# Kernel tuning notes

Measured on AMD Instinct MI355X. Metric: run time of the kernel, lower is better.

## Reference

```python
import jax, jax.numpy as jnp
import numpy as np

N_FFT = 2048
HOP = 512
N_FREQ = N_FFT // 2 + 1  # 1025


def _dft_conv_weights():
    # periodic ('fftbins=True') Hann window, matching librosa get_window('hann', N, fftbins=True)
    n = np.arange(N_FFT)
    win = 0.5 - 0.5 * np.cos(2.0 * np.pi * n / N_FFT)
    k = np.arange(N_FREQ)
    ang = 2.0 * np.pi * np.outer(k, n) / N_FFT  # (F, n_fft)
    # W[n, k] = exp(-2*pi*i*n*k/N); real part = cos, imag part = -sin; windowed per-tap
    w_real = (np.cos(ang) * win[None, :]).astype(np.float32)
    w_imag = (-np.sin(ang) * win[None, :]).astype(np.float32)
    return w_real, w_imag


def setup_inputs() -> dict:
    key = jax.random.key(0)
    x = jax.random.normal(key, (16, 320000), dtype=jnp.float32)
    w_real, w_imag = _dft_conv_weights()
    return {
        "input": x,
        "conv_real_w": jnp.asarray(w_real),
        "conv_imag_w": jnp.asarray(w_imag),
    }


def reference(input, conv_real_w, conv_imag_w):
    # center=True: reflect-pad n_fft//2 on both sides
    pad = N_FFT // 2
    x = jnp.pad(input, ((0, 0), (pad, pad)), mode="reflect")  # (B, L + n_fft)
    L = x.shape[1]
    T = (L - N_FFT) // HOP + 1  # time_steps
    # frame extraction == Conv1d with kernel n_fft, stride hop
    idx = jnp.arange(T)[:, None] * HOP + jnp.arange(N_FFT)[None, :]  # (T, n_fft)
    frames = x[:, idx]  # (B, T, n_fft)
    real = jnp.einsum("btn,fn->bft", frames, conv_real_w)  # (B, F, T)
    imag = jnp.einsum("btn,fn->bft", frames, conv_imag_w)  # (B, F, T)
    return real, imag
```

## Files before the change

kernel.cpp:

```cpp
#include <hip/hip_runtime.h>

#define B_BATCH 16
#define XLEN    320000
#define NFFT    2048
#define HOP     512
#define PADW    1024
#define NFREQ   1025
#define T_OUT   626
#define M_ROWS  2050
#define BM      128
#define BN      128
#define BK      64
#define MT      17
#define NTT     5
#define KT      32

#define XPAD_LEN    322048
#define XPAD_STRIDE 330240
#define APACK_BYTES ((size_t)MT * KT * 16384)
#define XPAD_BYTES  ((size_t)B_BATCH * XPAD_STRIDE * 2)
#define WS_NEEDED   (APACK_BYTES + XPAD_BYTES)

typedef __bf16 bf16x8 __attribute__((ext_vector_type(8)));
typedef __bf16 bf16x4 __attribute__((ext_vector_type(4)));
typedef float  f32x4  __attribute__((ext_vector_type(4)));

__device__ __forceinline__ unsigned lds_off(int row, int kbyte) {
    return (unsigned)(row * 128 + (kbyte ^ ((row & 7) << 4)));
}

__device__ __forceinline__ void gload_lds16(const void* g, void* l) {
    __builtin_amdgcn_global_load_lds(
        (const __attribute__((address_space(1))) unsigned int*)g,
        (__attribute__((address_space(3))) unsigned int*)l,
        16, 0, 0);
}

__global__ __launch_bounds__(256) void prep_w(
    const float* __restrict__ wre, const float* __restrict__ wim,
    __bf16* __restrict__ apack)
{
    const int gid  = blockIdx.x * 256 + threadIdx.x;
    const int slot = gid & 7;
    const int row  = (gid >> 3) & 127;
    const int kt   = (gid >> 10) & 31;
    const int mt   = gid >> 15;

    const int grow = mt * 128 + row;
    const int k    = kt * 64 + (slot ^ (row & 7)) * 8;

    bf16x8 v;
    if (grow < M_ROWS) {
        const float* src = (grow < NFREQ)
            ? (wre + (size_t)grow * NFFT + k)
            : (wim + (size_t)(grow - NFREQ) * NFFT + k);
        const float4 a = *reinterpret_cast<const float4*>(src);
        const float4 b = *reinterpret_cast<const float4*>(src + 4);
        v[0] = (__bf16)a.x; v[1] = (__bf16)a.y; v[2] = (__bf16)a.z; v[3] = (__bf16)a.w;
        v[4] = (__bf16)b.x; v[5] = (__bf16)b.y; v[6] = (__bf16)b.z; v[7] = (__bf16)b.w;
    } else {
        v = bf16x8{};
    }
    *reinterpret_cast<bf16x8*>(apack + ((size_t)(mt * KT + kt) * 8192 + row * 64 + slot * 8)) = v;
}

__global__ __launch_bounds__(256) void prep_x(
    const float* __restrict__ x, __bf16* __restrict__ xpad)
{
    const int gid = blockIdx.x * 256 + threadIdx.x;
    const int b   = gid / (XPAD_STRIDE / 8);
    const int i0  = (gid % (XPAD_STRIDE / 8)) * 8;
    const float* xb = x + (size_t)b * XLEN;

    bf16x8 v;
    const int pos0 = i0 - PADW;
    if (pos0 >= 0 && pos0 + 8 <= XLEN) {
        const float4 a = *reinterpret_cast<const float4*>(xb + pos0);
        const float4 c = *reinterpret_cast<const float4*>(xb + pos0 + 4);
        v[0] = (__bf16)a.x; v[1] = (__bf16)a.y; v[2] = (__bf16)a.z; v[3] = (__bf16)a.w;
        v[4] = (__bf16)c.x; v[5] = (__bf16)c.y; v[6] = (__bf16)c.z; v[7] = (__bf16)c.w;
    } else {
        #pragma unroll
        for (int e = 0; e < 8; ++e) {
            const int i = i0 + e;
            if (i >= XPAD_LEN) { v[e] = (__bf16)0.f; continue; }
            int p = i - PADW;
            p = (p < 0) ? -p : p;
            p = (p >= XLEN) ? (2 * XLEN - 2 - p) : p;
            v[e] = (__bf16)xb[p];
        }
    }
    *reinterpret_cast<bf16x8*>(xpad + (size_t)b * XPAD_STRIDE + i0) = v;
}

__global__ __launch_bounds__(256) void stft_gemm2(
    const __bf16* __restrict__ apack,
    const __bf16* __restrict__ xpad,
    float* __restrict__ out)
{
    __shared__ __align__(16) unsigned char ldsA[16384];
    __shared__ __align__(16) unsigned char ldsB[16384];

    const int tid  = threadIdx.x;
    const int lane = tid & 63;
    const int wid  = tid >> 6;
    const int wm   = wid >> 1;
    const int wn   = wid & 1;

    const int bid = blockIdx.x;
    const int b   = bid / (MT * NTT);
    const int rem = bid % (MT * NTT);
    const int mt  = rem / NTT;
    const int nt  = rem % NTT;

    const int row0 = mt * BM;
    const int col0 = nt * BN;

    const char* atiles = (const char*)(apack + (size_t)mt * KT * 8192);
    const char* xb     = (const char*)(xpad + (size_t)b * XPAD_STRIDE);

    const int br   = wid * 32 + (lane >> 3);
    const int bslt = lane & 7;
    const size_t boff_const = (size_t)(col0 + br) * 1024 + (size_t)((bslt ^ (br & 7)) * 16);

    f32x4 acc[4][4];
    #pragma unroll
    for (int m = 0; m < 4; ++m)
        #pragma unroll
        for (int n = 0; n < 4; ++n)
            acc[m][n] = f32x4{0.f, 0.f, 0.f, 0.f};

    const int fr = lane & 15;
    const int kq = lane >> 4;

    for (int kt = 0; kt < KT; ++kt) {
        const char* aglb = atiles + (size_t)kt * 16384 + wid * 4096 + lane * 16;
        #pragma unroll
        for (int i = 0; i < 4; ++i)
            gload_lds16(aglb + i * 1024, ldsA + wid * 4096 + i * 1024);

        const char* bglb = xb + boff_const + (size_t)kt * 128;
        #pragma unroll
        for (int i = 0; i < 4; ++i)
            gload_lds16(bglb + (size_t)i * 8192, ldsB + wid * 4096 + i * 1024);

        __syncthreads();

        #pragma unroll
        for (int kk = 0; kk < 2; ++kk) {
            const int kbyte = kk * 64 + kq * 16;
            bf16x8 af[4], bfv[4];
            #pragma unroll
            for (int m = 0; m < 4; ++m)
                af[m] = *reinterpret_cast<const bf16x8*>(
                    ldsA + lds_off(wm * 64 + m * 16 + fr, kbyte));
            #pragma unroll
            for (int n = 0; n < 4; ++n)
                bfv[n] = *reinterpret_cast<const bf16x8*>(
                    ldsB + lds_off(wn * 64 + n * 16 + fr, kbyte));
            #pragma unroll
            for (int m = 0; m < 4; ++m)
                #pragma unroll
                for (int n = 0; n < 4; ++n)
                    acc[m][n] = __builtin_amdgcn_mfma_f32_16x16x32_bf16(
                        af[m], bfv[n], acc[m][n], 0, 0, 0);
        }

        __syncthreads();
    }

    const size_t imag_base = (size_t)B_BATCH * NFREQ * T_OUT;
    #pragma unroll
    for (int m = 0; m < 4; ++m) {
        #pragma unroll
        for (int n = 0; n < 4; ++n) {
            #pragma unroll
            for (int j = 0; j < 4; ++j) {
                const int grow = row0 + wm * 64 + m * 16 + kq * 4 + j;
                const int gcol = col0 + wn * 64 + n * 16 + fr;
                if (grow < M_ROWS && gcol < T_OUT) {
                    size_t off;
                    if (grow < NFREQ)
                        off = ((size_t)b * NFREQ + grow) * T_OUT + gcol;
                    else
                        off = imag_base + ((size_t)b * NFREQ + (grow - NFREQ)) * T_OUT + gcol;
                    out[off] = acc[m][n][j];
                }
            }
        }
    }
}

__global__ __launch_bounds__(256) void stft_gemm_fb(
    const float* __restrict__ x,
    const float* __restrict__ wre,
    const float* __restrict__ wim,
    float* __restrict__ out)
{
    __shared__ __align__(16) unsigned char ldsA[BM * BK * 2];
    __shared__ __align__(16) unsigned char ldsB[BN * BK * 2];

    const int tid  = threadIdx.x;
    const int lane = tid & 63;
    const int wid  = tid >> 6;
    const int wm   = wid >> 1;
    const int wn   = wid & 1;

    const int bid = blockIdx.x;
    const int b   = bid / (MT * NTT);
    const int rem = bid % (MT * NTT);
    const int mt  = rem / NTT;
    const int nt  = rem % NTT;

    const int row0 = mt * BM;
    const int col0 = nt * BN;
    const float* xb = x + (size_t)b * XLEN;

    const int c4 = (tid & 15) * 4;
    const int r0 = tid >> 4;

    f32x4 acc[4][4];
    #pragma unroll
    for (int m = 0; m < 4; ++m)
        #pragma unroll
        for (int n = 0; n < 4; ++n)
            acc[m][n] = f32x4{0.f, 0.f, 0.f, 0.f};

    const int fr = lane & 15;
    const int kq = lane >> 4;

    for (int k0 = 0; k0 < NFFT; k0 += BK) {
        bf16x4 sa[8], sb[8];
        #pragma unroll
        for (int rr = 0; rr < 8; ++rr) {
            const int row  = rr * 16 + r0;
            const int grow = row0 + row;
            float4 v = make_float4(0.f, 0.f, 0.f, 0.f);
            if (grow < M_ROWS) {
                const float* wsrc = (grow < NFREQ)
                    ? (wre + (size_t)grow * NFFT)
                    : (wim + (size_t)(grow - NFREQ) * NFFT);
                v = *reinterpret_cast<const float4*>(wsrc + k0 + c4);
            }
            sa[rr].x = (__bf16)v.x; sa[rr].y = (__bf16)v.y;
            sa[rr].z = (__bf16)v.z; sa[rr].w = (__bf16)v.w;
        }
        #pragma unroll
        for (int rr = 0; rr < 8; ++rr) {
            const int trow = rr * 16 + r0;
            const int t    = col0 + trow;
            float4 v = make_float4(0.f, 0.f, 0.f, 0.f);
            if (t < T_OUT) {
                const int pos = t * HOP + k0 + c4 - PADW;
                if (pos >= 0 && pos <= XLEN - 4) {
                    v = *reinterpret_cast<const float4*>(xb + pos);
                } else {
                    float tmp[4];
                    #pragma unroll
                    for (int e = 0; e < 4; ++e) {
                        int p = pos + e;
                        p = (p < 0) ? -p : p;
                        p = (p >= XLEN) ? (2 * XLEN - 2 - p) : p;
                        tmp[e] = xb[p];
                    }
                    v = make_float4(tmp[0], tmp[1], tmp[2], tmp[3]);
                }
            }
            sb[rr].x = (__bf16)v.x; sb[rr].y = (__bf16)v.y;
            sb[rr].z = (__bf16)v.z; sb[rr].w = (__bf16)v.w;
        }
        __syncthreads();
        #pragma unroll
        for (int rr = 0; rr < 8; ++rr) {
            const int row = rr * 16 + r0;
            *reinterpret_cast<bf16x4*>(ldsA + lds_off(row, c4 * 2)) = sa[rr];
            *reinterpret_cast<bf16x4*>(ldsB + lds_off(row, c4 * 2)) = sb[rr];
        }
        __syncthreads();
        #pragma unroll
        for (int kk = 0; kk < 2; ++kk) {
            const int kbyte = kk * 64 + kq * 16;
            bf16x8 af[4], bfv[4];
            #pragma unroll
            for (int m = 0; m < 4; ++m)
                af[m] = *reinterpret_cast<const bf16x8*>(
                    ldsA + lds_off(wm * 64 + m * 16 + fr, kbyte));
            #pragma unroll
            for (int n = 0; n < 4; ++n)
                bfv[n] = *reinterpret_cast<const bf16x8*>(
                    ldsB + lds_off(wn * 64 + n * 16 + fr, kbyte));
            #pragma unroll
            for (int m = 0; m < 4; ++m)
                #pragma unroll
                for (int n = 0; n < 4; ++n)
                    acc[m][n] = __builtin_amdgcn_mfma_f32_16x16x32_bf16(
                        af[m], bfv[n], acc[m][n], 0, 0, 0);
        }
    }

    const size_t imag_base = (size_t)B_BATCH * NFREQ * T_OUT;
    #pragma unroll
    for (int m = 0; m < 4; ++m) {
        #pragma unroll
        for (int n = 0; n < 4; ++n) {
            #pragma unroll
            for (int j = 0; j < 4; ++j) {
                const int grow = row0 + wm * 64 + m * 16 + kq * 4 + j;
                const int gcol = col0 + wn * 64 + n * 16 + fr;
                if (grow < M_ROWS && gcol < T_OUT) {
                    size_t off;
                    if (grow < NFREQ)
                        off = ((size_t)b * NFREQ + grow) * T_OUT + gcol;
                    else
                        off = imag_base + ((size_t)b * NFREQ + (grow - NFREQ)) * T_OUT + gcol;
                    out[off] = acc[m][n][j];
                }
            }
        }
    }
}

extern "C" void kernel_launch(void* const* d_in, const int* in_sizes, int n_in,
                              void* d_out, int out_size, void* d_ws, size_t ws_size,
                              hipStream_t stream) {
    const float* x   = (const float*)d_in[0];
    const float* wre = (const float*)d_in[1];
    const float* wim = (const float*)d_in[2];
    float* out = (float*)d_out;

    if (ws_size < WS_NEEDED) {
        stft_gemm_fb<<<dim3(B_BATCH * MT * NTT), 256, 0, stream>>>(x, wre, wim, out);
        return;
    }

    __bf16* apack = (__bf16*)d_ws;
    __bf16* xpad  = (__bf16*)((char*)d_ws + APACK_BYTES);

    prep_w<<<dim3(MT * KT * 128 * 8 / 256), 256, 0, stream>>>(wre, wim, apack);
    prep_x<<<dim3(B_BATCH * (XPAD_STRIDE / 8) / 256), 256, 0, stream>>>(x, xpad);
    stft_gemm2<<<dim3(B_BATCH * MT * NTT), 256, 0, stream>>>(apack, xpad, out);
}
```

Baseline: 129.5 us.

## Rewrite STFT GEMM with 256-wide batch-flattened tiles and double-buffered LDS pipeline

Replaces the 128x128 single-buffered GEMM with a 512-thread, 128x256 tile kernel that treats batch and time as one flattened column dimension (16*626 columns), removing the per-batch padding waste of 5 column tiles per batch. A/B tiles are split into two 32-wide k-halves and staged through a double-buffered 96KB LDS ring using direct global-to-LDS loads, with explicit vmcnt waits, barriers and setprio to overlap loads with MFMA. Block indices are remapped for XCD-aware placement, the weight packing is re-laid-out with a 4-slot swizzle, and an extra zero batch row is padded to keep edge loads in bounds. The added complexity risks LDS occupancy limits and correctness of the hand-scheduled wait counts.

```diff
diff --git a/kernel.cpp b/kernel.cpp
--- a/kernel.cpp
+++ b/kernel.cpp
@@ -8,26 +8,23 @@
 #define NFREQ   1025
 #define T_OUT   626
 #define M_ROWS  2050
+#define NCOLS   (B_BATCH * T_OUT)
 #define BM      128
-#define BN      128
+#define BN      256
 #define BK      64
-#define MT      17
-#define NTT     5
-#define KT      32
+#define MT2     17
+#define NT2     40
+#define KT2     32
 
 #define XPAD_LEN    322048
 #define XPAD_STRIDE 330240
-#define APACK_BYTES ((size_t)MT * KT * 16384)
-#define XPAD_BYTES  ((size_t)B_BATCH * XPAD_STRIDE * 2)
+#define APACK_BYTES ((size_t)MT2 * KT2 * 2 * 8192)
+#define XPAD_BYTES  ((size_t)(B_BATCH + 1) * XPAD_STRIDE * 2)
 #define WS_NEEDED   (APACK_BYTES + XPAD_BYTES)
 
 typedef __bf16 bf16x8 __attribute__((ext_vector_type(8)));
 typedef __bf16 bf16x4 __attribute__((ext_vector_type(4)));
 typedef float  f32x4  __attribute__((ext_vector_type(4)));
-
-__device__ __forceinline__ unsigned lds_off(int row, int kbyte) {
-    return (unsigned)(row * 128 + (kbyte ^ ((row & 7) << 4)));
-}
 
 __device__ __forceinline__ void gload_lds16(const void* g, void* l) {
     __builtin_amdgcn_global_load_lds(
@@ -41,15 +38,16 @@
     __bf16* __restrict__ apack)
 {
     const int gid  = blockIdx.x * 256 + threadIdx.x;
-    const int slot = gid & 7;
-    const int row  = (gid >> 3) & 127;
-    const int kt   = (gid >> 10) & 31;
-    const int mt   = gid >> 15;
+    const int scell = gid & 3;
+    const int row   = (gid >> 2) & 127;
+    const int ks    = (gid >> 9) & 1;
+    const int kt    = (gid >> 10) & 31;
+    const int mt    = gid >> 15;
 
     const int grow = mt * 128 + row;
-    const int k    = kt * 64 + (slot ^ (row & 7)) * 8;
-
-    bf16x8 v;
+    const int k    = kt * 64 + ks * 32 + ((scell ^ (row & 3)) << 3);
+
+    bf16x8 v = bf16x8{};
     if (grow < M_ROWS) {
         const float* src = (grow < NFREQ)
             ? (wre + (size_t)grow * NFFT + k)
@@ -58,70 +56,138 @@
         const float4 b = *reinterpret_cast<const float4*>(src + 4);
         v[0] = (__bf16)a.x; v[1] = (__bf16)a.y; v[2] = (__bf16)a.z; v[3] = (__bf16)a.w;
         v[4] = (__bf16)b.x; v[5] = (__bf16)b.y; v[6] = (__bf16)b.z; v[7] = (__bf16)b.w;
-    } else {
-        v = bf16x8{};
-    }
-    *reinterpret_cast<bf16x8*>(apack + ((size_t)(mt * KT + kt) * 8192 + row * 64 + slot * 8)) = v;
+    }
+    *reinterpret_cast<bf16x8*>(apack + (size_t)gid * 8) = v;
 }
 
 __global__ __launch_bounds__(256) void prep_x(
     const float* __restrict__ x, __bf16* __restrict__ xpad)
 {
     const int gid = blockIdx.x * 256 + threadIdx.x;
-    const int b   = gid / (XPAD_STRIDE / 8);
-    const int i0  = (gid % (XPAD_STRIDE / 8)) * 8;
-    const float* xb = x + (size_t)b * XLEN;
-
-    bf16x8 v;
-    const int pos0 = i0 - PADW;
-    if (pos0 >= 0 && pos0 + 8 <= XLEN) {
-        const float4 a = *reinterpret_cast<const float4*>(xb + pos0);
-        const float4 c = *reinterpret_cast<const float4*>(xb + pos0 + 4);
-        v[0] = (__bf16)a.x; v[1] = (__bf16)a.y; v[2] = (__bf16)a.z; v[3] = (__bf16)a.w;
-        v[4] = (__bf16)c.x; v[5] = (__bf16)c.y; v[6] = (__bf16)c.z; v[7] = (__bf16)c.w;
-    } else {
-        #pragma unroll
-        for (int e = 0; e < 8; ++e) {
-            const int i = i0 + e;
-            if (i >= XPAD_LEN) { v[e] = (__bf16)0.f; continue; }
-            int p = i - PADW;
-            p = (p < 0) ? -p : p;
-            p = (p >= XLEN) ? (2 * XLEN - 2 - p) : p;
-            v[e] = (__bf16)xb[p];
+    if (gid >= (B_BATCH + 1) * (XPAD_STRIDE / 8)) return;
+    const int b  = gid / (XPAD_STRIDE / 8);
+    const int i0 = (gid - b * (XPAD_STRIDE / 8)) * 8;
+
+    bf16x8 v = bf16x8{};
+    if (b < B_BATCH) {
+        const float* xb = x + (size_t)b * XLEN;
+        const int pos0 = i0 - PADW;
+        if (pos0 >= 0 && pos0 + 8 <= XLEN) {
+            const float4 a = *reinterpret_cast<const float4*>(xb + pos0);
+            const float4 c = *reinterpret_cast<const float4*>(xb + pos0 + 4);
+            v[0] = (__bf16)a.x; v[1] = (__bf16)a.y; v[2] = (__bf16)a.z; v[3] = (__bf16)a.w;
+            v[4] = (__bf16)c.x; v[5] = (__bf16)c.y; v[6] = (__bf16)c.z; v[7] = (__bf16)c.w;
+        } else {
+            #pragma unroll
+            for (int e = 0; e < 8; ++e) {
+                const int i = i0 + e;
+                if (i >= XPAD_LEN) { v[e] = (__bf16)0.f; continue; }
+                int p = i - PADW;
+                p = (p < 0) ? -p : p;
+                p = (p >= XLEN) ? (2 * XLEN - 2 - p) : p;
+                v[e] = (__bf16)xb[p];
+            }
         }
     }
     *reinterpret_cast<bf16x8*>(xpad + (size_t)b * XPAD_STRIDE + i0) = v;
 }
 
-__global__ __launch_bounds__(256) void stft_gemm2(
+
+#define MFMA16 __builtin_amdgcn_mfma_f32_16x16x32_bf16
+
+#define PH(BUF, KS, STAGE, VMW) do {                                              \
+    const unsigned abase = (unsigned)(((BUF)*2+(KS)) << 13) + offA_base;          \
+    const unsigned bbase = (unsigned)(((BUF)*2+(KS)) << 14) + offB_base;          \
+    bf16x8 a0 = *(const bf16x8*)(lds + abase);                                    \
+    bf16x8 a1 = *(const bf16x8*)(lds + abase + 1024);                             \
+    bf16x8 a2 = *(const bf16x8*)(lds + abase + 2048);                             \
+    bf16x8 a3 = *(const bf16x8*)(lds + abase + 3072);                             \
+    bf16x8 b0 = *(const bf16x8*)(lds + bbase);                                    \
+    bf16x8 b1 = *(const bf16x8*)(lds + bbase + 1024);                             \
+    bf16x8 b2 = *(const bf16x8*)(lds + bbase + 2048);                             \
+    bf16x8 b3 = *(const bf16x8*)(lds + bbase + 3072);                             \
+    STAGE                                                                          \
+    VMW                                                                            \
+    __builtin_amdgcn_s_barrier();                                                  \
+    __builtin_amdgcn_s_setprio(1);                                                 \
+    acc[0][0] = MFMA16(a0, b0, acc[0][0], 0, 0, 0);                                \
+    acc[0][1] = MFMA16(a0, b1, acc[0][1], 0, 0, 0);                                \
+    acc[0][2] = MFMA16(a0, b2, acc[0][2], 0, 0, 0);                                \
+    acc[0][3] = MFMA16(a0, b3, acc[0][3], 0, 0, 0);                                \
+    acc[1][0] = MFMA16(a1, b0, acc[1][0], 0, 0, 0);                                \
+    acc[1][1] = MFMA16(a1, b1, acc[1][1], 0, 0, 0);                                \
+    acc[1][2] = MFMA16(a1, b2, acc[1][2], 0, 0, 0);                                \
+    acc[1][3] = MFMA16(a1, b3, acc[1][3], 0, 0, 0);                                \
+    acc[2][0] = MFMA16(a2, b0, acc[2][0], 0, 0, 0);                                \
+    acc[2][1] = MFMA16(a2, b1, acc[2][1], 0, 0, 0);                                \
+    acc[2][2] = MFMA16(a2, b2, acc[2][2], 0, 0, 0);                                \
+    acc[2][3] = MFMA16(a2, b3, acc[2][3], 0, 0, 0);                                \
+    acc[3][0] = MFMA16(a3, b0, acc[3][0], 0, 0, 0);                                \
+    acc[3][1] = MFMA16(a3, b1, acc[3][1], 0, 0, 0);                                \
+    acc[3][2] = MFMA16(a3, b2, acc[3][2], 0, 0, 0);                                \
+    acc[3][3] = MFMA16(a3, b3, acc[3][3], 0, 0, 0);                                \
+    __builtin_amdgcn_s_setprio(0);                                                 \
+    __builtin_amdgcn_s_barrier();                                                  \
+    __builtin_amdgcn_sched_barrier(0);                                             \
+} while (0)
+
+#define VM3 asm volatile("s_waitcnt vmcnt(3)" ::: "memory");
+#define VM0 asm volatile("s_waitcnt vmcnt(0)" ::: "memory");
+
+__global__ __launch_bounds__(512, 2) void stft_gemm3(
     const __bf16* __restrict__ apack,
     const __bf16* __restrict__ xpad,
     float* __restrict__ out)
 {
-    __shared__ __align__(16) unsigned char ldsA[16384];
-    __shared__ __align__(16) unsigned char ldsB[16384];
+    __shared__ __align__(16) unsigned char lds[98304];
 
     const int tid  = threadIdx.x;
     const int lane = tid & 63;
     const int wid  = tid >> 6;
-    const int wm   = wid >> 1;
-    const int wn   = wid & 1;
-
-    const int bid = blockIdx.x;
-    const int b   = bid / (MT * NTT);
-    const int rem = bid % (MT * NTT);
-    const int mt  = rem / NTT;
-    const int nt  = rem % NTT;
-
-    const int row0 = mt * BM;
-    const int col0 = nt * BN;
-
-    const char* atiles = (const char*)(apack + (size_t)mt * KT * 8192);
-    const char* xb     = (const char*)(xpad + (size_t)b * XPAD_STRIDE);
-
-    const int br   = wid * 32 + (lane >> 3);
-    const int bslt = lane & 7;
-    const size_t boff_const = (size_t)(col0 + br) * 1024 + (size_t)((bslt ^ (br & 7)) * 16);
+    const int wm   = wid >> 2;
+    const int wn   = wid & 3;
+    const int fr   = lane & 15;
+    const int kq   = lane >> 4;
+
+    const int orig = (blockIdx.x & 7) * 85 + (blockIdx.x >> 3);
+    const int nt = orig / MT2;
+    const int mt = orig % MT2;
+
+    const char* ablk = (const char*)apack + ((size_t)mt * KT2 * 2) * 8192 + (size_t)tid * 16;
+
+    const char* xpb = (const char*)xpad;
+    const int c0 = tid, c1 = tid + 512;
+    const char* gb0;
+    const char* gb1;
+    {
+        int row = c0 >> 2;
+        int col = nt * 256 + row;
+        unsigned b = (unsigned)col / 626u;
+        int tc = col - (int)b * 626;
+        int kqv = (c0 & 3) ^ (row & 3);
+        gb0 = xpb + ((size_t)b * XPAD_STRIDE + (size_t)tc * 512) * 2 + kqv * 16;
+        row = c1 >> 2;
+        col = nt * 256 + row;
+        b = (unsigned)col / 626u;
+        tc = col - (int)b * 626;
+        kqv = (c1 & 3) ^ (row & 3);
+        gb1 = xpb + ((size_t)b * XPAD_STRIDE + (size_t)tc * 512) * 2 + kqv * 16;
+    }
+
+    auto stageA = [&](int kt, int ks, int buf) {
+        gload_lds16(ablk + ((size_t)(kt * 2 + ks) << 13),
+                    lds + ((buf * 2 + ks) << 13) + (wid << 10));
+    };
+    auto stageB = [&](int kt, int ks, int buf) {
+        const int koff = kt * 128 + ks * 64;
+        unsigned char* d = lds + 32768 + ((buf * 2 + ks) << 14) + (wid << 10);
+        gload_lds16(gb0 + koff, d);
+        gload_lds16(gb1 + koff, d + 8192);
+    };
+
+    const unsigned swz = (unsigned)(((kq ^ fr) & 3) << 4);
+    const unsigned offA_base = (unsigned)((wm * 64 + fr) * 64) + swz;
+    const unsigned offB_base = 32768u + (unsigned)((wn * 64 + fr) * 64) + swz;
 
     f32x4 acc[4][4];
     #pragma unroll
@@ -130,65 +196,53 @@
         for (int n = 0; n < 4; ++n)
             acc[m][n] = f32x4{0.f, 0.f, 0.f, 0.f};
 
-    const int fr = lane & 15;
-    const int kq = lane >> 4;
-
-    for (int kt = 0; kt < KT; ++kt) {
-        const char* aglb = atiles + (size_t)kt * 16384 + wid * 4096 + lane * 16;
-        #pragma unroll
-        for (int i = 0; i < 4; ++i)
-            gload_lds16(aglb + i * 1024, ldsA + wid * 4096 + i * 1024);
-
-        const char* bglb = xb + boff_const + (size_t)kt * 128;
-        #pragma unroll
-        for (int i = 0; i < 4; ++i)
-            gload_lds16(bglb + (size_t)i * 8192, ldsB + wid * 4096 + i * 1024);
-
-        __syncthreads();
-
-        #pragma unroll
-        for (int kk = 0; kk < 2; ++kk) {
-            const int kbyte = kk * 64 + kq * 16;
-            bf16x8 af[4], bfv[4];
-            #pragma unroll
-            for (int m = 0; m < 4; ++m)
-                af[m] = *reinterpret_cast<const bf16x8*>(
-                    ldsA + lds_off(wm * 64 + m * 16 + fr, kbyte));
-            #pragma unroll
-            for (int n = 0; n < 4; ++n)
-                bfv[n] = *reinterpret_cast<const bf16x8*>(
-                    ldsB + lds_off(wn * 64 + n * 16 + fr, kbyte));
-            #pragma unroll
-            for (int m = 0; m < 4; ++m)
-                #pragma unroll
-                for (int n = 0; n < 4; ++n)
-                    acc[m][n] = __builtin_amdgcn_mfma_f32_16x16x32_bf16(
-                        af[m], bfv[n], acc[m][n], 0, 0, 0);
-        }
-
-        __syncthreads();
-    }
+    stageA(0, 0, 0); stageB(0, 0, 0);
+    stageA(0, 1, 0); stageB(0, 1, 0);
+    stageA(1, 0, 1); stageB(1, 0, 1);
+    VM3
+    __builtin_amdgcn_s_barrier();
+    __builtin_amdgcn_sched_barrier(0);
+
+    #pragma unroll 1
+    for (int i = 0; i < 15; ++i) {
+        const int t0 = 2 * i;
+        PH(0, 0, stageA(t0 + 1, 1, 1); stageB(t0 + 1, 1, 1);, );
+        PH(0, 1, stageA(t0 + 2, 0, 0); stageB(t0 + 2, 0, 0);, VM3);
+        PH(1, 0, stageA(t0 + 2, 1, 0); stageB(t0 + 2, 1, 0);, );
+        PH(1, 1, stageA(t0 + 3, 0, 1); stageB(t0 + 3, 0, 1);, VM3);
+    }
+    PH(0, 0, stageA(31, 1, 1); stageB(31, 1, 1);, );
+    PH(0, 1, , VM0);
+    PH(1, 0, , );
+    PH(1, 1, , );
 
     const size_t imag_base = (size_t)B_BATCH * NFREQ * T_OUT;
     #pragma unroll
-    for (int m = 0; m < 4; ++m) {
-        #pragma unroll
-        for (int n = 0; n < 4; ++n) {
-            #pragma unroll
-            for (int j = 0; j < 4; ++j) {
-                const int grow = row0 + wm * 64 + m * 16 + kq * 4 + j;
-                const int gcol = col0 + wn * 64 + n * 16 + fr;
-                if (grow < M_ROWS && gcol < T_OUT) {
-                    size_t off;
-                    if (grow < NFREQ)
-                        off = ((size_t)b * NFREQ + grow) * T_OUT + gcol;
-                    else
-                        off = imag_base + ((size_t)b * NFREQ + (grow - NFREQ)) * T_OUT + gcol;
-                    out[off] = acc[m][n][j];
+    for (int n = 0; n < 4; ++n) {
+        const int col = nt * 256 + wn * 64 + n * 16 + fr;
+        if (col < NCOLS) {
+            const unsigned b = (unsigned)col / 626u;
+            const int tc = col - (int)b * 626;
+            const size_t colbase = (size_t)b * NFREQ * T_OUT + (size_t)tc;
+            #pragma unroll
+            for (int m = 0; m < 4; ++m) {
+                #pragma unroll
+                for (int j = 0; j < 4; ++j) {
+                    const int grow = mt * 128 + wm * 64 + m * 16 + kq * 4 + j;
+                    if (grow < M_ROWS) {
+                        const size_t off = (grow < NFREQ)
+                            ? colbase + (size_t)grow * T_OUT
+                            : imag_base + colbase + (size_t)(grow - NFREQ) * T_OUT;
+                        out[off] = acc[m][n][j];
+                    }
                 }
             }
         }
     }
+}
+
+__device__ __forceinline__ unsigned lds_off_fb(int row, int kbyte) {
+    return (unsigned)(row * 128 + (kbyte ^ ((row & 7) << 4)));
 }
 
 __global__ __launch_bounds__(256) void stft_gemm_fb(
@@ -197,23 +251,23 @@
     const float* __restrict__ wim,
     float* __restrict__ out)
 {
-    __shared__ __align__(16) unsigned char ldsA[BM * BK * 2];
-    __shared__ __align__(16) unsigned char ldsB[BN * BK * 2];
+    __shared__ __align__(16) unsigned char ldsA[128 * 128];
+    __shared__ __align__(16) unsigned char ldsB[128 * 128];
 
     const int tid  = threadIdx.x;
     const int lane = tid & 63;
     const int wid  = tid >> 6;
-    const int wm   = wid >> 1;
-    const int wn   = wid & 1;
+    const int wmf  = wid >> 1;
+    const int wnf  = wid & 1;
 
     const int bid = blockIdx.x;
-    const int b   = bid / (MT * NTT);
-    const int rem = bid % (MT * NTT);
-    const int mt  = rem / NTT;
-    const int nt  = rem % NTT;
-
-    const int row0 = mt * BM;
-    const int col0 = nt * BN;
+    const int b   = bid / (17 * 5);
+    const int rem = bid % (17 * 5);
+    const int mt  = rem / 5;
+    const int nt  = rem % 5;
+
+    const int row0 = mt * 128;
+    const int col0 = nt * 128;
     const float* xb = x + (size_t)b * XLEN;
 
     const int c4 = (tid & 15) * 4;
@@ -229,7 +283,7 @@
     const int fr = lane & 15;
     const int kq = lane >> 4;
 
-    for (int k0 = 0; k0 < NFFT; k0 += BK) {
+    for (int k0 = 0; k0 < NFFT; k0 += 64) {
         bf16x4 sa[8], sb[8];
         #pragma unroll
         for (int rr = 0; rr < 8; ++rr) {
@@ -273,8 +327,8 @@
         #pragma unroll
         for (int rr = 0; rr < 8; ++rr) {
             const int row = rr * 16 + r0;
-            *reinterpret_cast<bf16x4*>(ldsA + lds_off(row, c4 * 2)) = sa[rr];
-            *reinterpret_cast<bf16x4*>(ldsB + lds_off(row, c4 * 2)) = sb[rr];
+            *reinterpret_cast<bf16x4*>(ldsA + lds_off_fb(row, c4 * 2)) = sa[rr];
+            *reinterpret_cast<bf16x4*>(ldsB + lds_off_fb(row, c4 * 2)) = sb[rr];
         }
         __syncthreads();
         #pragma unroll
@@ -284,17 +338,16 @@
             #pragma unroll
             for (int m = 0; m < 4; ++m)
                 af[m] = *reinterpret_cast<const bf16x8*>(
-                    ldsA + lds_off(wm * 64 + m * 16 + fr, kbyte));
+                    ldsA + lds_off_fb(wmf * 64 + m * 16 + fr, kbyte));
             #pragma unroll
             for (int n = 0; n < 4; ++n)
                 bfv[n] = *reinterpret_cast<const bf16x8*>(
-                    ldsB + lds_off(wn * 64 + n * 16 + fr, kbyte));
+                    ldsB + lds_off_fb(wnf * 64 + n * 16 + fr, kbyte));
             #pragma unroll
             for (int m = 0; m < 4; ++m)
                 #pragma unroll
                 for (int n = 0; n < 4; ++n)
-                    acc[m][n] = __builtin_amdgcn_mfma_f32_16x16x32_bf16(
-                        af[m], bfv[n], acc[m][n], 0, 0, 0);
+                    acc[m][n] = MFMA16(af[m], bfv[n], acc[m][n], 0, 0, 0);
         }
     }
 
@@ -305,8 +358,8 @@
         for (int n = 0; n < 4; ++n) {
             #pragma unroll
             for (int j = 0; j < 4; ++j) {
-                const int grow = row0 + wm * 64 + m * 16 + kq * 4 + j;
-                const int gcol = col0 + wn * 64 + n * 16 + fr;
+                const int grow = row0 + wmf * 64 + m * 16 + kq * 4 + j;
+                const int gcol = col0 + wnf * 64 + n * 16 + fr;
                 if (grow < M_ROWS && gcol < T_OUT) {
                     size_t off;
                     if (grow < NFREQ)
@@ -329,14 +382,14 @@
     float* out = (float*)d_out;
 
     if (ws_size < WS_NEEDED) {
-        stft_gemm_fb<<<dim3(B_BATCH * MT * NTT), 256, 0, stream>>>(x, wre, wim, out);
+        stft_gemm_fb<<<dim3(B_BATCH * 17 * 5), 256, 0, stream>>>(x, wre, wim, out);
         return;
     }
 
     __bf16* apack = (__bf16*)d_ws;
     __bf16* xpad  = (__bf16*)((char*)d_ws + APACK_BYTES);
 
-    prep_w<<<dim3(MT * KT * 128 * 8 / 256), 256, 0, stream>>>(wre, wim, apack);
-    prep_x<<<dim3(B_BATCH * (XPAD_STRIDE / 8) / 256), 256, 0, stream>>>(x, xpad);
-    stft_gemm2<<<dim3(B_BATCH * MT * NTT), 256, 0, stream>>>(apack, xpad, out);
-}
+    prep_w<<<dim3(557056 / 256), 256, 0, stream>>>(wre, wim, apack);
+    prep_x<<<dim3(((B_BATCH + 1) * (XPAD_STRIDE / 8) + 255) / 256), 256, 0, stream>>>(x, xpad);
+    stft_gemm3<<<dim3(MT2 * NT2), 512, 0, stream>>>(apack, xpad, out);
+}
```

Measured after the change: 135.8 us. +4.9%, slower.
